# Performance work log

Measured on AMD Instinct MI355X. Metric: run time of the kernel, lower is better.

The kernel has to match this reference:

```python
import jax, jax.numpy as jnp
import numpy as np

EMB_DIM = 1024
NUM_HEADS = 16
HEAD_SIZE = 64  # emb_dim // num_heads


def setup_inputs() -> dict:
    key = jax.random.key(0)
    k1, k2, k3 = jax.random.split(key, 3)
    B, T, C = 2, 2048, EMB_DIM
    x = jax.random.normal(k1, (B, T, C), dtype=jnp.float32)
    # Linear weights stored as (in, out); scale like PyTorch default init roughly
    W_qkv = jax.random.normal(k2, (C, 3 * C), dtype=jnp.float32) * (1.0 / np.sqrt(C))
    b_qkv = jnp.zeros((3 * C,), dtype=jnp.float32)
    W_out = jax.random.normal(k3, (C, C), dtype=jnp.float32) * (1.0 / np.sqrt(C))
    b_out = jnp.zeros((C,), dtype=jnp.float32)
    return {"x": x, "W_qkv": W_qkv, "b_qkv": b_qkv, "W_out": W_out, "b_out": b_out}


def reference(x, W_qkv, b_qkv, W_out, b_out):
    B, T, C = x.shape
    H, D = NUM_HEADS, HEAD_SIZE
    # QKV projection; torch views (B,T,3C) -> (B,T,3,H,D)
    qkv = (x @ W_qkv + b_qkv).reshape(B, T, 3, H, D)
    q, k, v = qkv[:, :, 0], qkv[:, :, 1], qkv[:, :, 2]  # each (B,T,H,D)
    # scores: (B,H,T,T), scaled by 1/sqrt(head_size)
    scores = jnp.einsum('bthd,bshd->bhts', q, k) / np.sqrt(D).astype(np.float32)
    causal = jnp.tril(jnp.ones((T, T), dtype=bool))
    scores = jnp.where(causal, scores, -jnp.inf)
    probs = jax.nn.softmax(scores, axis=-1)
    # weighted sum -> (B,T,H,D) -> (B,T,C)
    out = jnp.einsum('bhts,bshd->bthd', probs, v).reshape(B, T, C)
    return out @ W_out + b_out
```

## Files before the change

### kernel.cpp

```cpp
#include <hip/hip_runtime.h>
#include <hip/hip_bf16.h>
#include <cstdint>
#include <cstddef>

typedef unsigned short u16;
typedef __attribute__((ext_vector_type(8))) short bf16x8;
typedef __attribute__((ext_vector_type(4))) short bf16x4;
typedef __attribute__((ext_vector_type(4))) float f32x4;

#define AS1 __attribute__((address_space(1)))
#define AS3 __attribute__((address_space(3)))

static __device__ __forceinline__ u16 f2bf(float f) {
  union { float f; unsigned u; } c;
  c.f = f;
  unsigned r = c.u + 0x7fffu + ((c.u >> 16) & 1u);
  return (u16)(r >> 16);
}


__global__ __launch_bounds__(256) void cast_x_kernel(const float* __restrict__ in,
                                                     u16* __restrict__ out, int n4) {
  int i = blockIdx.x * blockDim.x + threadIdx.x;
  if (i < n4) {
    float4 v = reinterpret_cast<const float4*>(in)[i];
    ushort4 o;
    o.x = f2bf(v.x); o.y = f2bf(v.y); o.z = f2bf(v.z); o.w = f2bf(v.w);
    reinterpret_cast<ushort4*>(out)[i] = o;
  }
}

__global__ __launch_bounds__(256) void transpose_cast_kernel(const float* __restrict__ in,
                                                             u16* __restrict__ out,
                                                             int R, int C) {
  __shared__ float tile[32][33];
  int bx = blockIdx.x, by = blockIdx.y;
  int tx = threadIdx.x, ty = threadIdx.y;
  #pragma unroll
  for (int i = ty; i < 32; i += 8)
    tile[i][tx] = in[(size_t)(by * 32 + i) * C + bx * 32 + tx];
  __syncthreads();
  #pragma unroll
  for (int i = ty; i < 32; i += 8)
    out[(size_t)(bx * 32 + i) * R + by * 32 + tx] = f2bf(tile[tx][i]);
}

__global__ __launch_bounds__(512) void transpose_v_kernel(const u16* __restrict__ in,
                                                          u16* __restrict__ out) {
  __shared__ u16 tile[64][65];
  const int bh = blockIdx.y;
  const int t0 = blockIdx.x * 64;
  const int tx = threadIdx.x, ty = threadIdx.y;
  const u16* src = in + (size_t)bh * 2048 * 64;
  u16* dst = out + (size_t)bh * 64 * 2048;
  #pragma unroll
  for (int i = ty; i < 64; i += 8)
    tile[i][tx] = src[(size_t)(t0 + i) * 64 + tx];
  __syncthreads();
  #pragma unroll
  for (int i = ty; i < 64; i += 8)
    dst[(size_t)i * 2048 + t0 + tx] = tile[tx][i];
}

static __device__ __forceinline__ void gemm_mainloop(
    const u16* __restrict__ A, const u16* __restrict__ Bt, int K,
    int brow, int bcol, u16* lsA, u16* lsB, f32x4 acc[4][4]) {
  const int tid  = threadIdx.x;
  const int lane = tid & 63;
  const int wave = tid >> 6;
  const int wr = wave >> 1, wc = wave & 1;
  const int r = lane & 15, g = lane >> 4;

  for (int k0 = 0; k0 < K; k0 += 64) {
    #pragma unroll
    for (int i = 0; i < 4; ++i) {
      int chunk = i * 4 + wave;
      int e = (chunk * 64 + lane) * 8;
      int rr = e >> 6, cc = e & 63;
      __builtin_amdgcn_global_load_lds(
          (const AS1 void*)(A + (size_t)(brow + rr) * K + k0 + cc),
          (AS3 void*)(lsA + chunk * 512), 16, 0, 0);
      __builtin_amdgcn_global_load_lds(
          (const AS1 void*)(Bt + (size_t)(bcol + rr) * K + k0 + cc),
          (AS3 void*)(lsB + chunk * 512), 16, 0, 0);
    }
    __syncthreads();
    #pragma unroll
    for (int kk = 0; kk < 64; kk += 32) {
      bf16x8 af[4], bfr[4];
      #pragma unroll
      for (int m = 0; m < 4; ++m)
        af[m] = *reinterpret_cast<const bf16x8*>(lsA + (wr * 64 + m * 16 + r) * 64 + kk + g * 8);
      #pragma unroll
      for (int n = 0; n < 4; ++n)
        bfr[n] = *reinterpret_cast<const bf16x8*>(lsB + (wc * 64 + n * 16 + r) * 64 + kk + g * 8);
      #pragma unroll
      for (int m = 0; m < 4; ++m)
        #pragma unroll
        for (int n = 0; n < 4; ++n)
          acc[m][n] = __builtin_amdgcn_mfma_f32_16x16x32_bf16(af[m], bfr[n], acc[m][n], 0, 0, 0);
    }
    __syncthreads();
  }
}

__global__ __launch_bounds__(256) void gemm_qkv_kernel(
    const u16* __restrict__ A, const u16* __restrict__ Bt,
    const float* __restrict__ bias,
    u16* __restrict__ Qo, u16* __restrict__ Ko, u16* __restrict__ Vo) {
  __shared__ u16 lsA[128 * 64];
  __shared__ u16 lsB[128 * 64];
  f32x4 acc[4][4];
  #pragma unroll
  for (int m = 0; m < 4; ++m)
    #pragma unroll
    for (int n = 0; n < 4; ++n)
      acc[m][n] = (f32x4){0.f, 0.f, 0.f, 0.f};

  const int brow = blockIdx.y * 128;
  const int bcol = blockIdx.x * 128;
  gemm_mainloop(A, Bt, 1024, brow, bcol, lsA, lsB, acc);

  const float QSC = 0.125f * 1.44269504088896f;
  const int lane = threadIdx.x & 63;
  const int wave = threadIdx.x >> 6;
  const int wr = wave >> 1, wc = wave & 1;
  const int r = lane & 15, g = lane >> 4;
  #pragma unroll
  for (int n = 0; n < 4; ++n) {
    int col = bcol + wc * 64 + n * 16 + r;
    int s = col >> 10, h = (col >> 6) & 15, d = col & 63;
    float bv = bias[col];
    u16* dst = (s == 0) ? Qo : (s == 1) ? Ko : Vo;
    float sc = (s == 0) ? QSC : 1.f;
    #pragma unroll
    for (int m = 0; m < 4; ++m) {
      #pragma unroll
      for (int j = 0; j < 4; ++j) {
        int rowj = brow + wr * 64 + m * 16 + g * 4 + j;
        int b = rowj >> 11, t = rowj & 2047;
        dst[((size_t)(b * 16 + h) * 2048 + t) * 64 + d] = f2bf((acc[m][n][j] + bv) * sc);
      }
    }
  }
}

__global__ __launch_bounds__(256) void gemm_out_kernel(
    const u16* __restrict__ A, const u16* __restrict__ Bt,
    const float* __restrict__ bias, float* __restrict__ out) {
  __shared__ u16 lsA[128 * 64];
  __shared__ u16 lsB[128 * 64];
  f32x4 acc[4][4];
  #pragma unroll
  for (int m = 0; m < 4; ++m)
    #pragma unroll
    for (int n = 0; n < 4; ++n)
      acc[m][n] = (f32x4){0.f, 0.f, 0.f, 0.f};

  const int brow = blockIdx.y * 128;
  const int bcol = blockIdx.x * 128;
  gemm_mainloop(A, Bt, 1024, brow, bcol, lsA, lsB, acc);

  const int lane = threadIdx.x & 63;
  const int wave = threadIdx.x >> 6;
  const int wr = wave >> 1, wc = wave & 1;
  const int r = lane & 15, g = lane >> 4;
  #pragma unroll
  for (int n = 0; n < 4; ++n) {
    int col = bcol + wc * 64 + n * 16 + r;
    float bv = bias[col];
    #pragma unroll
    for (int m = 0; m < 4; ++m) {
      #pragma unroll
      for (int j = 0; j < 4; ++j) {
        int rowj = brow + wr * 64 + m * 16 + g * 4 + j;
        out[(size_t)rowj * 1024 + col] = acc[m][n][j] + bv;
      }
    }
  }
}

template<bool MASK>
static __device__ __forceinline__ void attn_tile_lds(
    int k0, int qw0, int lane,
    const u16* Kls, const u16* Vls,
    const bf16x8 (&qf)[2][2], f32x4 (&o)[2][4], float (&lsum)[2]) {
  const int r = lane & 15, g = lane >> 4;

  bf16x8 kf[4][2];
  #pragma unroll
  for (int kk = 0; kk < 4; ++kk) {
    int row = kk * 16 + r;
    int sw = row & 7;
    kf[kk][0] = *reinterpret_cast<const bf16x8*>(Kls + row * 64 + ((g ^ sw) * 8));
    kf[kk][1] = *reinterpret_cast<const bf16x8*>(Kls + row * 64 + (((g + 4) ^ sw) * 8));
  }
  bf16x4 vf[4][4];
  #pragma unroll
  for (int n = 0; n < 4; ++n) {
    int row = n * 16 + r;
    int sw = row & 7;
    #pragma unroll
    for (int kk = 0; kk < 4; ++kk) {
      int blk = (g >> 1) + kk * 2;
      vf[kk][n] = *reinterpret_cast<const bf16x4*>(
          Vls + row * 64 + ((blk ^ sw) * 8) + (g & 1) * 4);
    }
  }

  #pragma unroll
  for (int h2 = 0; h2 < 2; ++h2) {
    f32x4 st[4];
    #pragma unroll
    for (int kk = 0; kk < 4; ++kk) {
      st[kk] = (f32x4){0.f, 0.f, 0.f, 0.f};
      st[kk] = __builtin_amdgcn_mfma_f32_16x16x32_bf16(kf[kk][0], qf[h2][0], st[kk], 0, 0, 0);
      st[kk] = __builtin_amdgcn_mfma_f32_16x16x32_bf16(kf[kk][1], qf[h2][1], st[kk], 0, 0, 0);
    }
    const int q = qw0 + h2 * 16 + r;
    float p[16];
    #pragma unroll
    for (int kk = 0; kk < 4; ++kk)
      #pragma unroll
      for (int j = 0; j < 4; ++j) {
        float e = exp2f(st[kk][j]);
        p[kk * 4 + j] = (!MASK || (k0 + kk * 16 + g * 4 + j <= q)) ? e : 0.f;
      }
    float rs = 0.f;
    #pragma unroll
    for (int i = 0; i < 16; ++i) rs += p[i];
    lsum[h2] += rs;

    bf16x4 pf[4];
    #pragma unroll
    for (int kk = 0; kk < 4; ++kk)
      #pragma unroll
      for (int j = 0; j < 4; ++j)
        pf[kk][j] = (short)f2bf(p[kk * 4 + j]);

    #pragma unroll
    for (int n = 0; n < 4; ++n)
      #pragma unroll
      for (int kk = 0; kk < 4; ++kk)
        o[h2][n] = __builtin_amdgcn_mfma_f32_16x16x16bf16_1k(pf[kk], vf[kk][n], o[h2][n], 0, 0, 0);
  }
}

__global__ __launch_bounds__(256) void attn_kernel(
    const u16* __restrict__ Q, const u16* __restrict__ K,
    const u16* __restrict__ VT, u16* __restrict__ O) {
  __shared__ u16 Kls[2][64 * 64];
  __shared__ u16 Vls[2][64 * 64];

  const int tid  = threadIdx.x;
  const int lane = tid & 63;
  const int wave = tid >> 6;
  const int r = lane & 15, g = lane >> 4;
  const int bh = blockIdx.y;
  const int c = 15 - blockIdx.x;
  const int qw0 = c * 128 + wave * 32;
  const u16* Kp  = K  + (size_t)bh * 2048 * 64;
  const u16* VTp = VT + (size_t)bh * 64 * 2048;
  const u16* Qp  = Q  + (size_t)bh * 2048 * 64;

  bf16x8 qf[2][2];
  #pragma unroll
  for (int h2 = 0; h2 < 2; ++h2) {
    const u16* qp = Qp + (size_t)(qw0 + h2 * 16 + r) * 64 + g * 8;
    qf[h2][0] = *reinterpret_cast<const bf16x8*>(qp);
    qf[h2][1] = *reinterpret_cast<const bf16x8*>(qp + 32);
  }

  f32x4 o[2][4];
  #pragma unroll
  for (int h2 = 0; h2 < 2; ++h2)
    #pragma unroll
    for (int n = 0; n < 4; ++n) o[h2][n] = (f32x4){0.f, 0.f, 0.f, 0.f};
  float lsum[2] = {0.f, 0.f};

  auto stage = [&](int t, int buf) {
    const int k0s = t * 64;
    #pragma unroll
    for (int i = 0; i < 2; ++i) {
      int chunk = wave * 2 + i;
      int row = chunk * 8 + (lane >> 3);
      int blk = lane & 7;
      int off = ((blk ^ (row & 7)) * 8);
      __builtin_amdgcn_global_load_lds(
          (const AS1 void*)(Kp + (size_t)(k0s + row) * 64 + off),
          (AS3 void*)(&Kls[buf][chunk * 512]), 16, 0, 0);
      __builtin_amdgcn_global_load_lds(
          (const AS1 void*)(VTp + (size_t)row * 2048 + k0s + off),
          (AS3 void*)(&Vls[buf][chunk * 512]), 16, 0, 0);
    }
  };

  const int nT = 2 * c + 2;
  stage(0, 0);
  __syncthreads();
  int cur = 0;
  for (int t = 0; t < nT; ++t) {
    if (t + 1 < nT) stage(t + 1, cur ^ 1);
    if (t < nT - 2)
      attn_tile_lds<false>(t * 64, qw0, lane, Kls[cur], Vls[cur], qf, o, lsum);
    else
      attn_tile_lds<true>(t * 64, qw0, lane, Kls[cur], Vls[cur], qf, o, lsum);
    __syncthreads();
    cur ^= 1;
  }

  #pragma unroll
  for (int h2 = 0; h2 < 2; ++h2) {
    lsum[h2] += __shfl_xor(lsum[h2], 16);
    lsum[h2] += __shfl_xor(lsum[h2], 32);
  }

  const int b = bh >> 4, h = bh & 15;
  #pragma unroll
  for (int h2 = 0; h2 < 2; ++h2) {
    float linv[4];
    #pragma unroll
    for (int j = 0; j < 4; ++j)
      linv[j] = 1.f / __shfl(lsum[h2], (lane & 48) | (g * 4 + j));
    #pragma unroll
    for (int n = 0; n < 4; ++n) {
      #pragma unroll
      for (int j = 0; j < 4; ++j) {
        size_t row = (size_t)b * 2048 + qw0 + h2 * 16 + g * 4 + j;
        O[row * 1024 + h * 64 + n * 16 + r] = f2bf(o[h2][n][j] * linv[j]);
      }
    }
  }
}


extern "C" void kernel_launch(void* const* d_in, const int* in_sizes, int n_in,
                              void* d_out, int out_size, void* d_ws, size_t ws_size,
                              hipStream_t stream) {
  const float* x    = (const float*)d_in[0];
  const float* Wqkv = (const float*)d_in[1];
  const float* bqkv = (const float*)d_in[2];
  const float* Wout = (const float*)d_in[3];
  const float* bout = (const float*)d_in[4];
  float* out = (float*)d_out;

  char* p = (char*)d_ws;
  u16* xbf   = (u16*)p; p += (size_t)4096 * 1024 * 2;
  u16* wqkvT = (u16*)p; p += (size_t)3072 * 1024 * 2;
  u16* woutT = (u16*)p; p += (size_t)1024 * 1024 * 2;
  u16* Qb    = (u16*)p; p += (size_t)32 * 2048 * 64 * 2;
  u16* Kb    = (u16*)p; p += (size_t)32 * 2048 * 64 * 2;
  u16* Vb    = (u16*)p; p += (size_t)32 * 2048 * 64 * 2;
  u16* Vt    = (u16*)p; p += (size_t)32 * 64 * 2048 * 2;
  u16* attn  = xbf;

  cast_x_kernel<<<4096, 256, 0, stream>>>(x, xbf, 4096 * 1024 / 4);
  transpose_cast_kernel<<<dim3(96, 32), dim3(32, 8), 0, stream>>>(Wqkv, wqkvT, 1024, 3072);
  transpose_cast_kernel<<<dim3(32, 32), dim3(32, 8), 0, stream>>>(Wout, woutT, 1024, 1024);
  gemm_qkv_kernel<<<dim3(24, 32), 256, 0, stream>>>(xbf, wqkvT, bqkv, Qb, Kb, Vb);
  transpose_v_kernel<<<dim3(32, 32), dim3(64, 8), 0, stream>>>(Vb, Vt);
  attn_kernel<<<dim3(16, 32), 256, 0, stream>>>(Qb, Kb, Vt, attn);
  gemm_out_kernel<<<dim3(8, 32), 256, 0, stream>>>(attn, woutT, bout, out);
}
```

Before: 246.8 us.

## Swizzle GEMM block order, shrink out-GEMM tiles, split attention into smaller blocks

Remaps the QKV GEMM block index so neighbouring workgroups share A/B tiles, which is meant to improve L2 reuse. The output GEMM uses 128x64 tiles with its own single-buffered main loop and a similar swizzle, doubling the grid from 256 to 512 blocks to fill more CUs. The attention kernel drops to 2 waves per block covering 64 query rows, doubling the block count (1024) so the causal work is spread more evenly. The cost is more redundant K/V staging and a simpler, non-pipelined out-GEMM loop.

```diff
diff --git a/kernel.cpp b/kernel.cpp
--- a/kernel.cpp
+++ b/kernel.cpp
@@ -117,8 +117,10 @@
     for (int n = 0; n < 4; ++n)
       acc[m][n] = (f32x4){0.f, 0.f, 0.f, 0.f};
 
-  const int brow = blockIdx.y * 128;
-  const int bcol = blockIdx.x * 128;
+  const int lin = blockIdx.y * 24 + blockIdx.x;
+  const int nl  = (lin & 7) * 96 + (lin >> 3);
+  const int brow = (nl / 24) * 128;
+  const int bcol = (nl % 24) * 128;
   gemm_mainloop(A, Bt, 1024, brow, bcol, lsA, lsB, acc);
 
   const float QSC = 0.125f * 1.44269504088896f;
@@ -149,31 +151,71 @@
     const u16* __restrict__ A, const u16* __restrict__ Bt,
     const float* __restrict__ bias, float* __restrict__ out) {
   __shared__ u16 lsA[128 * 64];
-  __shared__ u16 lsB[128 * 64];
-  f32x4 acc[4][4];
-  #pragma unroll
-  for (int m = 0; m < 4; ++m)
+  __shared__ u16 lsB[64 * 64];
+  f32x4 acc[2][4];
+  #pragma unroll
+  for (int m = 0; m < 2; ++m)
     #pragma unroll
     for (int n = 0; n < 4; ++n)
       acc[m][n] = (f32x4){0.f, 0.f, 0.f, 0.f};
 
-  const int brow = blockIdx.y * 128;
-  const int bcol = blockIdx.x * 128;
-  gemm_mainloop(A, Bt, 1024, brow, bcol, lsA, lsB, acc);
-
-  const int lane = threadIdx.x & 63;
-  const int wave = threadIdx.x >> 6;
-  const int wr = wave >> 1, wc = wave & 1;
+  const int lin = blockIdx.y * 16 + blockIdx.x;
+  const int nl  = (lin & 7) * 64 + (lin >> 3);
+  const int brow = (nl / 16) * 128;
+  const int bcol = (nl % 16) * 64;
+
+  const int tid  = threadIdx.x;
+  const int lane = tid & 63;
+  const int wave = tid >> 6;
   const int r = lane & 15, g = lane >> 4;
+
+  for (int k0 = 0; k0 < 1024; k0 += 64) {
+    #pragma unroll
+    for (int i = 0; i < 6; ++i) {
+      int chunk = wave * 6 + i;
+      if (chunk < 16) {
+        int e = (chunk * 64 + lane) * 8;
+        int rr = e >> 6, cc = e & 63;
+        __builtin_amdgcn_global_load_lds(
+            (const AS1 void*)(A + (size_t)(brow + rr) * 1024 + k0 + cc),
+            (AS3 void*)(lsA + chunk * 512), 16, 0, 0);
+      } else {
+        int ch = chunk - 16;
+        int e = (ch * 64 + lane) * 8;
+        int rr = e >> 6, cc = e & 63;
+        __builtin_amdgcn_global_load_lds(
+            (const AS1 void*)(Bt + (size_t)(bcol + rr) * 1024 + k0 + cc),
+            (AS3 void*)(lsB + ch * 512), 16, 0, 0);
+      }
+    }
+    __syncthreads();
+    #pragma unroll
+    for (int kk = 0; kk < 64; kk += 32) {
+      bf16x8 af[2], bfr[4];
+      #pragma unroll
+      for (int m = 0; m < 2; ++m)
+        af[m] = *reinterpret_cast<const bf16x8*>(lsA + (wave * 32 + m * 16 + r) * 64 + kk + g * 8);
+      #pragma unroll
+      for (int n = 0; n < 4; ++n)
+        bfr[n] = *reinterpret_cast<const bf16x8*>(lsB + (n * 16 + r) * 64 + kk + g * 8);
+      #pragma unroll
+      for (int m = 0; m < 2; ++m)
+        #pragma unroll
+        for (int n = 0; n < 4; ++n)
+          acc[m][n] = __builtin_amdgcn_mfma_f32_16x16x32_bf16(af[m], bfr[n], acc[m][n], 0, 0, 0);
+    }
+    __syncthreads();
+  }
+
   #pragma unroll
   for (int n = 0; n < 4; ++n) {
-    int col = bcol + wc * 64 + n * 16 + r;
+    int col = bcol + n * 16 + r;
     float bv = bias[col];
     #pragma unroll
-    for (int m = 0; m < 4; ++m) {
+    for (int m = 0; m < 2; ++m) {
       #pragma unroll
       for (int j = 0; j < 4; ++j) {
-        int rowj = brow + wr * 64 + m * 16 + g * 4 + j;
+        int rowj = brow + wave * 32 + m * 16 + g * 4 + j;
         out[(size_t)rowj * 1024 + col] = acc[m][n][j] + bv;
       }
     }
@@ -246,7 +288,7 @@
   }
 }
 
-__global__ __launch_bounds__(256) void attn_kernel(
+__global__ __launch_bounds__(128) void attn_kernel(
     const u16* __restrict__ Q, const u16* __restrict__ K,
     const u16* __restrict__ VT, u16* __restrict__ O) {
   __shared__ u16 Kls[2][64 * 64];
@@ -257,8 +299,8 @@
   const int wave = tid >> 6;
   const int r = lane & 15, g = lane >> 4;
   const int bh = blockIdx.y;
-  const int c = 15 - blockIdx.x;
-  const int qw0 = c * 128 + wave * 32;
+  const int c = 31 - blockIdx.x;
+  const int qw0 = c * 64 + wave * 32;
   const u16* Kp  = K  + (size_t)bh * 2048 * 64;
   const u16* VTp = VT + (size_t)bh * 64 * 2048;
   const u16* Qp  = Q  + (size_t)bh * 2048 * 64;
@@ -281,8 +323,8 @@
   auto stage = [&](int t, int buf) {
     const int k0s = t * 64;
     #pragma unroll
-    for (int i = 0; i < 2; ++i) {
-      int chunk = wave * 2 + i;
+    for (int i = 0; i < 4; ++i) {
+      int chunk = wave * 4 + i;
       int row = chunk * 8 + (lane >> 3);
       int blk = lane & 7;
       int off = ((blk ^ (row & 7)) * 8);
@@ -295,13 +337,13 @@
     }
   };
 
-  const int nT = 2 * c + 2;
+  const int nT = c + 1;
   stage(0, 0);
   __syncthreads();
   int cur = 0;
   for (int t = 0; t < nT; ++t) {
     if (t + 1 < nT) stage(t + 1, cur ^ 1);
-    if (t < nT - 2)
+    if (t < nT - 1)
       attn_tile_lds<false>(t * 64, qw0, lane, Kls[cur], Vls[cur], qf, o, lsum);
     else
       attn_tile_lds<true>(t * 64, qw0, lane, Kls[cur], Vls[cur], qf, o, lsum);
@@ -359,6 +401,6 @@
   transpose_cast_kernel<<<dim3(32, 32), dim3(32, 8), 0, stream>>>(Wout, woutT, 1024, 1024);
   gemm_qkv_kernel<<<dim3(24, 32), 256, 0, stream>>>(xbf, wqkvT, bqkv, Qb, Kb, Vb);
   transpose_v_kernel<<<dim3(32, 32), dim3(64, 8), 0, stream>>>(Vb, Vt);
-  attn_kernel<<<dim3(16, 32), 256, 0, stream>>>(Qb, Kb, Vt, attn);
-  gemm_out_kernel<<<dim3(8, 32), 256, 0, stream>>>(attn, woutT, bout, out);
-}
+  attn_kernel<<<dim3(32, 32), 128, 0, stream>>>(Qb, Kb, Vt, attn);
+  gemm_out_kernel<<<dim3(16, 32), 256, 0, stream>>>(attn, woutT, bout, out);
+}
```

Result: slower. 252.7 us (+2.4%).
